# Kernel tuning notes

Hardware: AMD Instinct MI355X
Metric: run time of the kernel (lower is better)

## Reference

```python
import jax, jax.numpy as jnp
import numpy as np
from jax import lax

N_KERNELS = 10000
KS = 9
DILATIONS = (1, 2, 4, 8, 16)   # static dilation groups, 2000 kernels each
GROUP = N_KERNELS // len(DILATIONS)
BN_EPS = 1e-5


def setup_inputs() -> dict:
    key = jax.random.key(0)
    kx, kw, kb, klw = jax.random.split(key, 4)
    B, L, C, n_class = 16, 256, 3, 10
    x_enc = jax.random.normal(kx, (B, L, C), dtype=jnp.float32)
    # ROCKET kernels: normal weights, mean-centered per kernel
    W = jax.random.normal(kw, (N_KERNELS, C, KS), dtype=jnp.float32)
    W = W - W.mean(axis=(1, 2), keepdims=True)
    # ROCKET biases: uniform(-1, 1)
    b = jax.random.uniform(kb, (N_KERNELS,), dtype=jnp.float32) * 2.0 - 1.0
    gamma = jnp.ones((2 * N_KERNELS,), dtype=jnp.float32)
    beta = jnp.zeros((2 * N_KERNELS,), dtype=jnp.float32)
    linW = jax.random.normal(klw, (2 * N_KERNELS, n_class), dtype=jnp.float32) * 0.01
    linB = jnp.zeros((n_class,), dtype=jnp.float32)
    return {"x_enc": x_enc, "W": W, "b": b, "gamma": gamma, "beta": beta,
            "linW": linW, "linB": linB}


def _rocket_features(x, W, b):
    # x: [B, C, L]; W: [N_KERNELS, C, KS]; b: [N_KERNELS]
    feats = []
    dn = ("NCH", "OIH", "NCH")
    for i, d in enumerate(DILATIONS):
        w = W[i * GROUP:(i + 1) * GROUP]                       # [G, C, KS]
        bb = b[i * GROUP:(i + 1) * GROUP]                      # [G]
        y = lax.conv_general_dilated(x, w, window_strides=(1,),
                                     padding="SAME", rhs_dilation=(d,),
                                     dimension_numbers=dn)      # [B, G, L]
        y = y + bb[None, :, None]
        feats.append(y.max(axis=-1))                            # max pooling
        feats.append(jnp.where(y > 0, 1.0, 0.0).mean(axis=-1))  # PPV
    return jnp.concatenate(feats, axis=-1)                      # [B, 2*N_KERNELS]


def reference(x_enc, W, b, gamma, beta, linW, linB):
    x = jnp.transpose(x_enc, (0, 2, 1))        # [B, C, L]
    feat = _rocket_features(x, W, b)           # [B, 20000]
    # BatchNorm1d (training mode: batch statistics, biased variance)
    mu = feat.mean(axis=0)
    var = feat.var(axis=0)
    feat_n = (feat - mu) * lax.rsqrt(var + BN_EPS) * gamma + beta
    return feat_n @ linW + linB                # [B, num_class]
```

## Files before the change

kernel.cpp:

```cpp
#include <hip/hip_runtime.h>
#include <cmath>

#define NK       10000
#define GROUP    2000
#define SEQ_L    256
#define FEAT_DIM 20000
#define NBATCH   16
#define NSLICE   160

typedef _Float16 half8 __attribute__((ext_vector_type(8)));
typedef float    f32x4 __attribute__((ext_vector_type(4)));

__launch_bounds__(256)
__global__ void conv_feat(const float* __restrict__ x_enc,
                          const float* __restrict__ Wk,
                          const float* __restrict__ bias,
                          float* __restrict__ feat)
{
    __shared__ __align__(16) _Float16 Bh[1024 * 8];
    __shared__ __align__(16) _Float16 Bl[1024 * 8];

    const int mt  = blockIdx.x;
    const int gi  = blockIdx.y;
    const int b   = blockIdx.z;
    const int d   = 1 << gi;
    const int tid = threadIdx.x;
    const int l   = tid & 63;
    const int wv  = tid >> 6;
    const int kb  = l >> 4;
    const int lr  = l & 15;

    half8 ahi[4], alo[4];
#pragma unroll
    for (int tt = 0; tt < 4; ++tt) {
        const int nl = mt * 256 + wv * 64 + tt * 16 + lr;
        const int n  = gi * GROUP + (nl < GROUP ? nl : GROUP - 1);
#pragma unroll
        for (int j = 0; j < 8; ++j) {
            const int k = kb * 8 + j;
            float w;
            if (k < 27)       w = Wk[n * 27 + k];
            else if (k == 27) w = bias[n];
            else              w = 0.f;
            const _Float16 h = (_Float16)w;
            ahi[tt][j] = h;
            alo[tt][j] = (_Float16)(w - (float)h);
        }
    }

#pragma unroll
    for (int q = 0; q < 4; ++q) {
        half8 hv, lv;
#pragma unroll
        for (int kk = 0; kk < 8; ++kk) {
            const int k2 = q * 8 + kk;
            float v = 0.f;
            if (k2 < 27) {
                const int c  = k2 / 9;
                const int k9 = k2 - c * 9;
                const int t2 = tid + (k9 - 4) * d;
                if (t2 >= 0 && t2 < SEQ_L)
                    v = x_enc[(b * SEQ_L + t2) * 3 + c];
            } else if (k2 == 27) {
                v = 1.0f;
            }
            const _Float16 h = (_Float16)v;
            hv[kk] = h;
            lv[kk] = (_Float16)(v - (float)h);
        }
        *(half8*)&Bh[(q * 256 + tid) * 8] = hv;
        *(half8*)&Bl[(q * 256 + tid) * 8] = lv;
    }
    __syncthreads();

    float mx[4][4];
    int   cnt[4][4];
#pragma unroll
    for (int tt = 0; tt < 4; ++tt)
#pragma unroll
        for (int r = 0; r < 4; ++r) { mx[tt][r] = -INFINITY; cnt[tt][r] = 0; }

#pragma unroll
    for (int ch = 0; ch < 16; ++ch) {
        const int t = ch * 16 + lr;
        const half8 bh = *(const half8*)&Bh[(kb * 256 + t) * 8];
        const half8 bl = *(const half8*)&Bl[(kb * 256 + t) * 8];
#pragma unroll
        for (int tt = 0; tt < 4; ++tt) {
            f32x4 acc = {0.f, 0.f, 0.f, 0.f};
            acc = __builtin_amdgcn_mfma_f32_16x16x32_f16(ahi[tt], bh, acc, 0, 0, 0);
            acc = __builtin_amdgcn_mfma_f32_16x16x32_f16(alo[tt], bh, acc, 0, 0, 0);
            acc = __builtin_amdgcn_mfma_f32_16x16x32_f16(ahi[tt], bl, acc, 0, 0, 0);
#pragma unroll
            for (int r = 0; r < 4; ++r) {
                const float y = acc[r];
                mx[tt][r]   = fmaxf(mx[tt][r], y);
                cnt[tt][r] += (y > 0.f) ? 1 : 0;
            }
        }
    }

#pragma unroll
    for (int tt = 0; tt < 4; ++tt)
#pragma unroll
        for (int r = 0; r < 4; ++r) {
#pragma unroll
            for (int m = 1; m < 16; m <<= 1) {
                mx[tt][r]   = fmaxf(mx[tt][r], __shfl_xor(mx[tt][r], m));
                cnt[tt][r] += __shfl_xor(cnt[tt][r], m);
            }
        }

    if (lr == 0) {
        float* fb = feat + b * FEAT_DIM + gi * 4000;
#pragma unroll
        for (int tt = 0; tt < 4; ++tt)
#pragma unroll
            for (int r = 0; r < 4; ++r) {
                const int nl = mt * 256 + wv * 64 + tt * 16 + kb * 4 + r;
                if (nl < GROUP) {
                    fb[nl]        = mx[tt][r];
                    fb[2000 + nl] = (float)cnt[tt][r] * (1.0f / 256.0f);
                }
            }
    }
}

__launch_bounds__(256)
__global__ void bn_gemv_final(const float* __restrict__ feat,
                              const float* __restrict__ gamma,
                              const float* __restrict__ beta,
                              const float* __restrict__ linW,
                              const float* __restrict__ linB,
                              float* __restrict__ partial,
                              unsigned* __restrict__ counter,
                              float* __restrict__ out)
{
    __shared__ float gs[125], hs[125];
    __shared__ float lw[125 * 10];
    __shared__ int   lastflag;
    const int sl  = blockIdx.x;
    const int f0  = sl * 125;
    const int tid = threadIdx.x;

    for (int i = tid; i < 1250; i += 256) lw[i] = linW[f0 * 10 + i];

    if (tid < 125) {
        const int f = f0 + tid;
        float s = 0.f, ss = 0.f;
#pragma unroll
        for (int b = 0; b < NBATCH; ++b) {
            const float v = feat[b * FEAT_DIM + f];
            s += v; ss += v * v;
        }
        const float mu  = s * (1.f / NBATCH);
        const float var = ss * (1.f / NBATCH) - mu * mu;
        const float gg  = gamma[f] * rsqrtf(var + 1e-5f);
        gs[tid] = gg;
        hs[tid] = beta[f] - mu * gg;
    }
    __syncthreads();

    const int bb = tid >> 4;
    const int ft = tid & 15;
    float acc[10];
#pragma unroll
    for (int c = 0; c < 10; ++c) acc[c] = 0.f;

    for (int i = ft; i < 125; i += 16) {
        const float tv = fmaf(feat[bb * FEAT_DIM + f0 + i], gs[i], hs[i]);
#pragma unroll
        for (int c = 0; c < 10; ++c) acc[c] = fmaf(tv, lw[i * 10 + c], acc[c]);
    }
#pragma unroll
    for (int c = 0; c < 10; ++c)
#pragma unroll
        for (int m = 1; m < 16; m <<= 1) acc[c] += __shfl_xor(acc[c], m);

    if (ft == 0) {
#pragma unroll
        for (int c = 0; c < 10; ++c)
            partial[(sl * NBATCH + bb) * 10 + c] = acc[c];
    }

    __syncthreads();
    if (tid == 0) {
        __threadfence();
        const unsigned old =
            __hip_atomic_fetch_add(counter, 1u, __ATOMIC_ACQ_REL,
                                   __HIP_MEMORY_SCOPE_AGENT);
        lastflag = (old == NSLICE - 1);
    }
    __syncthreads();

    if (lastflag) {
        __threadfence();
        if (tid < 160) {
            float s = linB[tid % 10];
            for (int q = 0; q < NSLICE; ++q)
                s += __hip_atomic_load(&partial[q * 160 + tid],
                                       __ATOMIC_RELAXED,
                                       __HIP_MEMORY_SCOPE_AGENT);
            out[tid] = s;
        }
    }
}

extern "C" void kernel_launch(void* const* d_in, const int* in_sizes, int n_in,
                              void* d_out, int out_size, void* d_ws, size_t ws_size,
                              hipStream_t stream) {
    const float* x     = (const float*)d_in[0];
    const float* Wk    = (const float*)d_in[1];
    const float* bias  = (const float*)d_in[2];
    const float* gamma = (const float*)d_in[3];
    const float* beta  = (const float*)d_in[4];
    const float* linW  = (const float*)d_in[5];
    const float* linB  = (const float*)d_in[6];
    float* out = (float*)d_out;

    float*    feat    = (float*)d_ws;
    float*    partial = feat + NBATCH * FEAT_DIM;
    unsigned* counter = (unsigned*)(partial + NSLICE * 160);

    hipMemsetAsync(counter, 0, sizeof(unsigned), stream);
    conv_feat<<<dim3(8, 5, NBATCH), 256, 0, stream>>>(x, Wk, bias, feat);
    bn_gemv_final<<<dim3(NSLICE), 256, 0, stream>>>(feat, gamma, beta, linW,
                                                    linB, partial, counter, out);
}
```

Measured before the change: 42.85 us.

## Precompute im2col B operand once per dilation/batch in a separate kernel

```diff
diff --git a/kernel.cpp b/kernel.cpp
--- a/kernel.cpp
+++ b/kernel.cpp
@@ -6,24 +6,73 @@
 #define SEQ_L    256
 #define FEAT_DIM 20000
 #define NBATCH   16
-#define NSLICE   160
+#define NSLICE   40
+#define SLICE_F  500
 
 typedef _Float16 half8 __attribute__((ext_vector_type(8)));
 typedef float    f32x4 __attribute__((ext_vector_type(4)));
 
 __launch_bounds__(256)
-__global__ void conv_feat(const float* __restrict__ x_enc,
+__global__ void build_B(const float* __restrict__ x_enc,
+                        _Float16* __restrict__ Bh_g,
+                        _Float16* __restrict__ Bl_g,
+                        unsigned* __restrict__ counter)
+{
+    __shared__ __align__(16) float xp[3 * 384];
+    const int gi  = blockIdx.x;
+    const int b   = blockIdx.y;
+    const int d   = 1 << gi;
+    const int tid = threadIdx.x;
+
+    if (gi == 0 && b == 0 && tid == 0)
+        __hip_atomic_store(counter, 0u, __ATOMIC_RELEASE, __HIP_MEMORY_SCOPE_AGENT);
+
+    for (int i = tid; i < 3 * 384; i += 256) xp[i] = 0.f;
+    __syncthreads();
+    for (int e = tid; e < SEQ_L * 3; e += 256) {
+        const int t = e / 3;
+        const int c = e - t * 3;
+        xp[c * 384 + 64 + t] = x_enc[(b * SEQ_L + t) * 3 + c];
+    }
+    __syncthreads();
+
+    const int base = (gi * NBATCH + b) * 1024;
+#pragma unroll
+    for (int q = 0; q < 4; ++q) {
+        const int idx = q * 256 + tid;
+        const int kb  = idx >> 8;
+        const int t   = idx & 255;
+        half8 hv, lv;
+#pragma unroll
+        for (int kk = 0; kk < 8; ++kk) {
+            const int k2 = kb * 8 + kk;
+            float v = 0.f;
+            if (k2 < 27) {
+                const int c  = (k2 >= 18) ? 2 : (k2 >= 9 ? 1 : 0);
+                const int k9 = k2 - c * 9;
+                v = xp[c * 384 + 64 + t + (k9 - 4) * d];
+            } else if (k2 == 27) {
+                v = 1.0f;
+            }
+            const _Float16 h = (_Float16)v;
+            hv[kk] = h;
+            lv[kk] = (_Float16)(v - (float)h);
+        }
+        *(half8*)&Bh_g[(base + idx) * 8] = hv;
+        *(half8*)&Bl_g[(base + idx) * 8] = lv;
+    }
+}
+
+__launch_bounds__(128)
+__global__ void gemm_feat(const _Float16* __restrict__ Bh_g,
+                          const _Float16* __restrict__ Bl_g,
                           const float* __restrict__ Wk,
                           const float* __restrict__ bias,
                           float* __restrict__ feat)
 {
-    __shared__ __align__(16) _Float16 Bh[1024 * 8];
-    __shared__ __align__(16) _Float16 Bl[1024 * 8];
-
     const int mt  = blockIdx.x;
     const int gi  = blockIdx.y;
     const int b   = blockIdx.z;
-    const int d   = 1 << gi;
     const int tid = threadIdx.x;
     const int l   = tid & 63;
     const int wv  = tid >> 6;
@@ -33,7 +82,7 @@
     half8 ahi[4], alo[4];
 #pragma unroll
     for (int tt = 0; tt < 4; ++tt) {
-        const int nl = mt * 256 + wv * 64 + tt * 16 + lr;
+        const int nl = mt * 128 + wv * 64 + tt * 16 + lr;
         const int n  = gi * GROUP + (nl < GROUP ? nl : GROUP - 1);
 #pragma unroll
         for (int j = 0; j < 8; ++j) {
@@ -48,30 +97,8 @@
         }
     }
 
-#pragma unroll
-    for (int q = 0; q < 4; ++q) {
-        half8 hv, lv;
-#pragma unroll
-        for (int kk = 0; kk < 8; ++kk) {
-            const int k2 = q * 8 + kk;
-            float v = 0.f;
-            if (k2 < 27) {
-                const int c  = k2 / 9;
-                const int k9 = k2 - c * 9;
-                const int t2 = tid + (k9 - 4) * d;
-                if (t2 >= 0 && t2 < SEQ_L)
-                    v = x_enc[(b * SEQ_L + t2) * 3 + c];
-            } else if (k2 == 27) {
-                v = 1.0f;
-            }
-            const _Float16 h = (_Float16)v;
-            hv[kk] = h;
-            lv[kk] = (_Float16)(v - (float)h);
-        }
-        *(half8*)&Bh[(q * 256 + tid) * 8] = hv;
-        *(half8*)&Bl[(q * 256 + tid) * 8] = lv;
-    }
-    __syncthreads();
+    const _Float16* bhp = Bh_g + ((gi * NBATCH + b) * 1024 + kb * 256) * 8;
+    const _Float16* blp = Bl_g + ((gi * NBATCH + b) * 1024 + kb * 256) * 8;
 
     float mx[4][4];
     int   cnt[4][4];
@@ -83,8 +110,8 @@
 #pragma unroll
     for (int ch = 0; ch < 16; ++ch) {
         const int t = ch * 16 + lr;
-        const half8 bh = *(const half8*)&Bh[(kb * 256 + t) * 8];
-        const half8 bl = *(const half8*)&Bl[(kb * 256 + t) * 8];
+        const half8 bh = *(const half8*)&bhp[t * 8];
+        const half8 bl = *(const half8*)&blp[t * 8];
 #pragma unroll
         for (int tt = 0; tt < 4; ++tt) {
             f32x4 acc = {0.f, 0.f, 0.f, 0.f};
@@ -117,7 +144,7 @@
         for (int tt = 0; tt < 4; ++tt)
 #pragma unroll
             for (int r = 0; r < 4; ++r) {
-                const int nl = mt * 256 + wv * 64 + tt * 16 + kb * 4 + r;
+                const int nl = mt * 128 + wv * 64 + tt * 16 + kb * 4 + r;
                 if (nl < GROUP) {
                     fb[nl]        = mx[tt][r];
                     fb[2000 + nl] = (float)cnt[tt][r] * (1.0f / 256.0f);
@@ -136,17 +163,17 @@
                               unsigned* __restrict__ counter,
                               float* __restrict__ out)
 {
-    __shared__ float gs[125], hs[125];
-    __shared__ float lw[125 * 10];
+    __shared__ float gs[SLICE_F], hs[SLICE_F];
+    __shared__ float lw[SLICE_F * 10];
     __shared__ int   lastflag;
     const int sl  = blockIdx.x;
-    const int f0  = sl * 125;
+    const int f0  = sl * SLICE_F;
     const int tid = threadIdx.x;
 
-    for (int i = tid; i < 1250; i += 256) lw[i] = linW[f0 * 10 + i];
-
-    if (tid < 125) {
-        const int f = f0 + tid;
+    for (int i = tid; i < SLICE_F * 10; i += 256) lw[i] = linW[f0 * 10 + i];
+
+    for (int i = tid; i < SLICE_F; i += 256) {
+        const int f = f0 + i;
         float s = 0.f, ss = 0.f;
 #pragma unroll
         for (int b = 0; b < NBATCH; ++b) {
@@ -156,8 +183,8 @@
         const float mu  = s * (1.f / NBATCH);
         const float var = ss * (1.f / NBATCH) - mu * mu;
         const float gg  = gamma[f] * rsqrtf(var + 1e-5f);
-        gs[tid] = gg;
-        hs[tid] = beta[f] - mu * gg;
+        gs[i] = gg;
+        hs[i] = beta[f] - mu * gg;
     }
     __syncthreads();
 
@@ -167,7 +194,7 @@
 #pragma unroll
     for (int c = 0; c < 10; ++c) acc[c] = 0.f;
 
-    for (int i = ft; i < 125; i += 16) {
+    for (int i = ft; i < SLICE_F; i += 16) {
         const float tv = fmaf(feat[bb * FEAT_DIM + f0 + i], gs[i], hs[i]);
 #pragma unroll
         for (int c = 0; c < 10; ++c) acc[c] = fmaf(tv, lw[i * 10 + c], acc[c]);
@@ -197,6 +224,7 @@
         __threadfence();
         if (tid < 160) {
             float s = linB[tid % 10];
+#pragma unroll
             for (int q = 0; q < NSLICE; ++q)
                 s += __hip_atomic_load(&partial[q * 160 + tid],
                                        __ATOMIC_RELAXED,
@@ -221,9 +249,11 @@
     float*    feat    = (float*)d_ws;
     float*    partial = feat + NBATCH * FEAT_DIM;
     unsigned* counter = (unsigned*)(partial + NSLICE * 160);
-
-    hipMemsetAsync(counter, 0, sizeof(unsigned), stream);
-    conv_feat<<<dim3(8, 5, NBATCH), 256, 0, stream>>>(x, Wk, bias, feat);
+    _Float16* Bh      = (_Float16*)(counter + 4);
+    _Float16* Bl      = Bh + 5 * NBATCH * 1024 * 8;
+
+    build_B<<<dim3(5, NBATCH), 256, 0, stream>>>(x, Bh, Bl, counter);
+    gemm_feat<<<dim3(16, 5, NBATCH), 128, 0, stream>>>(Bh, Bl, Wk, bias, feat);
     bn_gemv_final<<<dim3(NSLICE), 256, 0, stream>>>(feat, gamma, beta, linW,
                                                     linB, partial, counter, out);
 }
```

New measurement: 38.60 us. -9.9%, faster.

## Fuse conv and BN-GEMV kernels into one launch with atomic-counter handoff

Applied to the files above, without the earlier changes.

```diff
diff --git a/kernel.cpp b/kernel.cpp
--- a/kernel.cpp
+++ b/kernel.cpp
@@ -1,207 +1,229 @@
 #include <hip/hip_runtime.h>
 #include <cmath>
 
-#define NK       10000
-#define GROUP    2000
-#define SEQ_L    256
-#define FEAT_DIM 20000
-#define NBATCH   16
-#define NSLICE   160
+#define NK        10000
+#define GROUP     2000
+#define SEQ_L     256
+#define FEAT_DIM  20000
+#define NBATCH    16
+#define CONV_BLKS 640
+#define NSLICE    40
+#define SLICE_F   500
+#define TOTAL_BLKS (CONV_BLKS + NSLICE)
 
 typedef _Float16 half8 __attribute__((ext_vector_type(8)));
 typedef float    f32x4 __attribute__((ext_vector_type(4)));
 
 __launch_bounds__(256)
-__global__ void conv_feat(const float* __restrict__ x_enc,
+__global__ void fused_all(const float* __restrict__ x_enc,
                           const float* __restrict__ Wk,
                           const float* __restrict__ bias,
-                          float* __restrict__ feat)
+                          const float* __restrict__ gamma,
+                          const float* __restrict__ beta,
+                          const float* __restrict__ linW,
+                          const float* __restrict__ linB,
+                          float* __restrict__ feat,
+                          float* __restrict__ partial,
+                          unsigned* __restrict__ counters,
+                          float* __restrict__ out)
 {
-    __shared__ __align__(16) _Float16 Bh[1024 * 8];
-    __shared__ __align__(16) _Float16 Bl[1024 * 8];
-
-    const int mt  = blockIdx.x;
-    const int gi  = blockIdx.y;
-    const int b   = blockIdx.z;
-    const int d   = 1 << gi;
+    __shared__ __align__(16) char smem[32768 + 16];
+    const int bid = blockIdx.x;
     const int tid = threadIdx.x;
-    const int l   = tid & 63;
-    const int wv  = tid >> 6;
-    const int kb  = l >> 4;
-    const int lr  = l & 15;
-
-    half8 ahi[4], alo[4];
-#pragma unroll
-    for (int tt = 0; tt < 4; ++tt) {
-        const int nl = mt * 256 + wv * 64 + tt * 16 + lr;
-        const int n  = gi * GROUP + (nl < GROUP ? nl : GROUP - 1);
-#pragma unroll
-        for (int j = 0; j < 8; ++j) {
-            const int k = kb * 8 + j;
-            float w;
-            if (k < 27)       w = Wk[n * 27 + k];
-            else if (k == 27) w = bias[n];
-            else              w = 0.f;
-            const _Float16 h = (_Float16)w;
-            ahi[tt][j] = h;
-            alo[tt][j] = (_Float16)(w - (float)h);
-        }
-    }
-
-#pragma unroll
-    for (int q = 0; q < 4; ++q) {
-        half8 hv, lv;
-#pragma unroll
-        for (int kk = 0; kk < 8; ++kk) {
-            const int k2 = q * 8 + kk;
-            float v = 0.f;
-            if (k2 < 27) {
-                const int c  = k2 / 9;
-                const int k9 = k2 - c * 9;
-                const int t2 = tid + (k9 - 4) * d;
-                if (t2 >= 0 && t2 < SEQ_L)
-                    v = x_enc[(b * SEQ_L + t2) * 3 + c];
-            } else if (k2 == 27) {
-                v = 1.0f;
-            }
-            const _Float16 h = (_Float16)v;
-            hv[kk] = h;
-            lv[kk] = (_Float16)(v - (float)h);
-        }
-        *(half8*)&Bh[(q * 256 + tid) * 8] = hv;
-        *(half8*)&Bl[(q * 256 + tid) * 8] = lv;
-    }
-    __syncthreads();
-
-    float mx[4][4];
-    int   cnt[4][4];
-#pragma unroll
-    for (int tt = 0; tt < 4; ++tt)
-#pragma unroll
-        for (int r = 0; r < 4; ++r) { mx[tt][r] = -INFINITY; cnt[tt][r] = 0; }
-
-#pragma unroll
-    for (int ch = 0; ch < 16; ++ch) {
-        const int t = ch * 16 + lr;
-        const half8 bh = *(const half8*)&Bh[(kb * 256 + t) * 8];
-        const half8 bl = *(const half8*)&Bl[(kb * 256 + t) * 8];
+
+    if (bid < CONV_BLKS) {
+        _Float16* Bh = (_Float16*)smem;
+        _Float16* Bl = (_Float16*)(smem + 16384);
+
+        const int mt = bid / 80;
+        const int rr = bid - mt * 80;
+        const int gi = rr >> 4;
+        const int b  = rr & 15;
+        const int d  = 1 << gi;
+        const int l  = tid & 63;
+        const int wv = tid >> 6;
+        const int kb = l >> 4;
+        const int lr = l & 15;
+
+        half8 ahi[4], alo[4];
 #pragma unroll
         for (int tt = 0; tt < 4; ++tt) {
-            f32x4 acc = {0.f, 0.f, 0.f, 0.f};
-            acc = __builtin_amdgcn_mfma_f32_16x16x32_f16(ahi[tt], bh, acc, 0, 0, 0);
-            acc = __builtin_amdgcn_mfma_f32_16x16x32_f16(alo[tt], bh, acc, 0, 0, 0);
-            acc = __builtin_amdgcn_mfma_f32_16x16x32_f16(ahi[tt], bl, acc, 0, 0, 0);
+            const int nl = mt * 256 + wv * 64 + tt * 16 + lr;
+            const int n  = gi * GROUP + (nl < GROUP ? nl : GROUP - 1);
+#pragma unroll
+            for (int j = 0; j < 8; ++j) {
+                const int k = kb * 8 + j;
+                float w;
+                if (k < 27)       w = Wk[n * 27 + k];
+                else if (k == 27) w = bias[n];
+                else              w = 0.f;
+                const _Float16 h = (_Float16)w;
+                ahi[tt][j] = h;
+                alo[tt][j] = (_Float16)(w - (float)h);
+            }
+        }
+
+#pragma unroll
+        for (int q = 0; q < 4; ++q) {
+            half8 hv, lv;
+#pragma unroll
+            for (int kk = 0; kk < 8; ++kk) {
+                const int k2 = q * 8 + kk;
+                float v = 0.f;
+                if (k2 < 27) {
+                    const int c  = k2 / 9;
+                    const int k9 = k2 - c * 9;
+                    const int t2 = tid + (k9 - 4) * d;
+                    if (t2 >= 0 && t2 < SEQ_L)
+                        v = x_enc[(b * SEQ_L + t2) * 3 + c];
+                } else if (k2 == 27) {
+                    v = 1.0f;
+                }
+                const _Float16 h = (_Float16)v;
+                hv[kk] = h;
+                lv[kk] = (_Float16)(v - (float)h);
+            }
+            *(half8*)&Bh[(q * 256 + tid) * 8] = hv;
+            *(half8*)&Bl[(q * 256 + tid) * 8] = lv;
+        }
+        __syncthreads();
+
+        float mx[4][4];
+        int   cnt[4][4];
+#pragma unroll
+        for (int tt = 0; tt < 4; ++tt)
+#pragma unroll
+            for (int r = 0; r < 4; ++r) { mx[tt][r] = -INFINITY; cnt[tt][r] = 0; }
+
+#pragma unroll
+        for (int ch = 0; ch < 16; ++ch) {
+            const int t = ch * 16 + lr;
+            const half8 bh = *(const half8*)&Bh[(kb * 256 + t) * 8];
+            const half8 bl = *(const half8*)&Bl[(kb * 256 + t) * 8];
+#pragma unroll
+            for (int tt = 0; tt < 4; ++tt) {
+                f32x4 acc = {0.f, 0.f, 0.f, 0.f};
+                acc = __builtin_amdgcn_mfma_f32_16x16x32_f16(ahi[tt], bh, acc, 0, 0, 0);
+                acc = __builtin_amdgcn_mfma_f32_16x16x32_f16(alo[tt], bh, acc, 0, 0, 0);
+                acc = __builtin_amdgcn_mfma_f32_16x16x32_f16(ahi[tt], bl, acc, 0, 0, 0);
+#pragma unroll
+                for (int r = 0; r < 4; ++r) {
+                    const float y = acc[r];
+                    mx[tt][r]   = fmaxf(mx[tt][r], y);
+                    cnt[tt][r] += (y > 0.f) ? 1 : 0;
+                }
+            }
+        }
+
+#pragma unroll
+        for (int tt = 0; tt < 4; ++tt)
 #pragma unroll
             for (int r = 0; r < 4; ++r) {
-                const float y = acc[r];
-                mx[tt][r]   = fmaxf(mx[tt][r], y);
-                cnt[tt][r] += (y > 0.f) ? 1 : 0;
-            }
-        }
-    }
-
-#pragma unroll
-    for (int tt = 0; tt < 4; ++tt)
-#pragma unroll
-        for (int r = 0; r < 4; ++r) {
-#pragma unroll
-            for (int m = 1; m < 16; m <<= 1) {
-                mx[tt][r]   = fmaxf(mx[tt][r], __shfl_xor(mx[tt][r], m));
-                cnt[tt][r] += __shfl_xor(cnt[tt][r], m);
-            }
-        }
-
-    if (lr == 0) {
-        float* fb = feat + b * FEAT_DIM + gi * 4000;
-#pragma unroll
-        for (int tt = 0; tt < 4; ++tt)
-#pragma unroll
-            for (int r = 0; r < 4; ++r) {
-                const int nl = mt * 256 + wv * 64 + tt * 16 + kb * 4 + r;
-                if (nl < GROUP) {
-                    fb[nl]        = mx[tt][r];
-                    fb[2000 + nl] = (float)cnt[tt][r] * (1.0f / 256.0f);
-                }
-            }
-    }
-}
-
-__launch_bounds__(256)
-__global__ void bn_gemv_final(const float* __restrict__ feat,
-                              const float* __restrict__ gamma,
-                              const float* __restrict__ beta,
-                              const float* __restrict__ linW,
-                              const float* __restrict__ linB,
-                              float* __restrict__ partial,
-                              unsigned* __restrict__ counter,
-                              float* __restrict__ out)
-{
-    __shared__ float gs[125], hs[125];
-    __shared__ float lw[125 * 10];
-    __shared__ int   lastflag;
-    const int sl  = blockIdx.x;
-    const int f0  = sl * 125;
-    const int tid = threadIdx.x;
-
-    for (int i = tid; i < 1250; i += 256) lw[i] = linW[f0 * 10 + i];
-
-    if (tid < 125) {
-        const int f = f0 + tid;
-        float s = 0.f, ss = 0.f;
-#pragma unroll
-        for (int b = 0; b < NBATCH; ++b) {
-            const float v = feat[b * FEAT_DIM + f];
-            s += v; ss += v * v;
-        }
-        const float mu  = s * (1.f / NBATCH);
-        const float var = ss * (1.f / NBATCH) - mu * mu;
-        const float gg  = gamma[f] * rsqrtf(var + 1e-5f);
-        gs[tid] = gg;
-        hs[tid] = beta[f] - mu * gg;
-    }
-    __syncthreads();
-
-    const int bb = tid >> 4;
-    const int ft = tid & 15;
-    float acc[10];
-#pragma unroll
-    for (int c = 0; c < 10; ++c) acc[c] = 0.f;
-
-    for (int i = ft; i < 125; i += 16) {
-        const float tv = fmaf(feat[bb * FEAT_DIM + f0 + i], gs[i], hs[i]);
-#pragma unroll
-        for (int c = 0; c < 10; ++c) acc[c] = fmaf(tv, lw[i * 10 + c], acc[c]);
-    }
-#pragma unroll
-    for (int c = 0; c < 10; ++c)
-#pragma unroll
-        for (int m = 1; m < 16; m <<= 1) acc[c] += __shfl_xor(acc[c], m);
-
-    if (ft == 0) {
+#pragma unroll
+                for (int m = 1; m < 16; m <<= 1) {
+                    mx[tt][r]   = fmaxf(mx[tt][r], __shfl_xor(mx[tt][r], m));
+                    cnt[tt][r] += __shfl_xor(cnt[tt][r], m);
+                }
+            }
+
+        if (lr == 0) {
+            float* fb = feat + b * FEAT_DIM + gi * 4000;
+#pragma unroll
+            for (int tt = 0; tt < 4; ++tt)
+#pragma unroll
+                for (int r = 0; r < 4; ++r) {
+                    const int nl = mt * 256 + wv * 64 + tt * 16 + kb * 4 + r;
+                    if (nl < GROUP) {
+                        fb[nl]        = mx[tt][r];
+                        fb[2000 + nl] = (float)cnt[tt][r] * (1.0f / 256.0f);
+                    }
+                }
+        }
+
+        __syncthreads();
+        if (tid == 0) {
+            __threadfence();
+            __hip_atomic_fetch_add(&counters[0], 1u, __ATOMIC_RELEASE,
+                                   __HIP_MEMORY_SCOPE_AGENT);
+        }
+    } else {
+        float* gs  = (float*)smem;
+        float* hs  = gs + SLICE_F;
+        float* lw  = hs + SLICE_F;
+        int*   flg = (int*)(smem + 24064);
+
+        const int sl = bid - CONV_BLKS;
+        const int f0 = sl * SLICE_F;
+
+        if (tid == 0) {
+            while (__hip_atomic_load(&counters[0], __ATOMIC_ACQUIRE,
+                                     __HIP_MEMORY_SCOPE_AGENT) < CONV_BLKS)
+                __builtin_amdgcn_s_sleep(32);
+            __threadfence();
+        }
+        __syncthreads();
+
+        for (int i = tid; i < SLICE_F * 10; i += 256) lw[i] = linW[f0 * 10 + i];
+
+        for (int i = tid; i < SLICE_F; i += 256) {
+            const int f = f0 + i;
+            float s = 0.f, ss = 0.f;
+#pragma unroll
+            for (int b = 0; b < NBATCH; ++b) {
+                const float v = feat[b * FEAT_DIM + f];
+                s += v; ss += v * v;
+            }
+            const float mu  = s * (1.f / NBATCH);
+            const float var = ss * (1.f / NBATCH) - mu * mu;
+            const float gg  = gamma[f] * rsqrtf(var + 1e-5f);
+            gs[i] = gg;
+            hs[i] = beta[f] - mu * gg;
+        }
+        __syncthreads();
+
+        const int bb = tid >> 4;
+        const int ft = tid & 15;
+        float acc[10];
+#pragma unroll
+        for (int c = 0; c < 10; ++c) acc[c] = 0.f;
+
+        for (int i = ft; i < SLICE_F; i += 16) {
+            const float tv = fmaf(feat[bb * FEAT_DIM + f0 + i], gs[i], hs[i]);
+#pragma unroll
+            for (int c = 0; c < 10; ++c) acc[c] = fmaf(tv, lw[i * 10 + c], acc[c]);
+        }
 #pragma unroll
         for (int c = 0; c < 10; ++c)
-            partial[(sl * NBATCH + bb) * 10 + c] = acc[c];
-    }
-
-    __syncthreads();
-    if (tid == 0) {
-        __threadfence();
-        const unsigned old =
-            __hip_atomic_fetch_add(counter, 1u, __ATOMIC_ACQ_REL,
-                                   __HIP_MEMORY_SCOPE_AGENT);
-        lastflag = (old == NSLICE - 1);
-    }
-    __syncthreads();
-
-    if (lastflag) {
-        __threadfence();
-        if (tid < 160) {
-            float s = linB[tid % 10];
-            for (int q = 0; q < NSLICE; ++q)
-                s += __hip_atomic_load(&partial[q * 160 + tid],
-                                       __ATOMIC_RELAXED,
+#pragma unroll
+            for (int m = 1; m < 16; m <<= 1) acc[c] += __shfl_xor(acc[c], m);
+
+        if (ft == 0) {
+#pragma unroll
+            for (int c = 0; c < 10; ++c)
+                partial[(sl * NBATCH + bb) * 10 + c] = acc[c];
+        }
+
+        __syncthreads();
+        if (tid == 0) {
+            __threadfence();
+            const unsigned old =
+                __hip_atomic_fetch_add(&counters[1], 1u, __ATOMIC_ACQ_REL,
                                        __HIP_MEMORY_SCOPE_AGENT);
-            out[tid] = s;
+            *flg = (old == NSLICE - 1);
+        }
+        __syncthreads();
+
+        if (*flg) {
+            __threadfence();
+            if (tid < 160) {
+                float s = linB[tid % 10];
+#pragma unroll
+                for (int q = 0; q < NSLICE; ++q)
+                    s += __hip_atomic_load(&partial[q * 160 + tid],
+                                           __ATOMIC_RELAXED,
+                                           __HIP_MEMORY_SCOPE_AGENT);
+                out[tid] = s;
+            }
         }
     }
 }
@@ -218,12 +240,12 @@
     const float* linB  = (const float*)d_in[6];
     float* out = (float*)d_out;
 
-    float*    feat    = (float*)d_ws;
-    float*    partial = feat + NBATCH * FEAT_DIM;
-    unsigned* counter = (unsigned*)(partial + NSLICE * 160);
-
-    hipMemsetAsync(counter, 0, sizeof(unsigned), stream);
-    conv_feat<<<dim3(8, 5, NBATCH), 256, 0, stream>>>(x, Wk, bias, feat);
-    bn_gemv_final<<<dim3(NSLICE), 256, 0, stream>>>(feat, gamma, beta, linW,
-                                                    linB, partial, counter, out);
+    float*    feat     = (float*)d_ws;
+    float*    partial  = feat + NBATCH * FEAT_DIM;
+    unsigned* counters = (unsigned*)(partial + NSLICE * 160);
+
+    hipMemsetAsync(counters, 0, 2 * sizeof(unsigned), stream);
+    fused_all<<<dim3(TOTAL_BLKS), 256, 0, stream>>>(x, Wk, bias, gamma, beta,
+                                                    linW, linB, feat, partial,
+                                                    counters, out);
 }
```

Measured after the change: 69.61 us. 62.4% more time.
